# Kernel optimization log

Hardware: AMD Instinct MI355X
Metric: run time of the kernel (lower is better)

## Reference

```python
import jax, jax.numpy as jnp
import numpy as np

B, N, DIN = 16, 1024, 256
HEADS, OUT_DIM = 4, 256
F = OUT_DIM // HEADS  # per-head feature dim
NEG_SLOPE = 0.2
MASK_VAL = -1e9


def setup_inputs() -> dict:
    key = jax.random.key(0)
    k1, k2, k3, k4, k5, k6 = jax.random.split(key, 6)
    x = jax.random.normal(k1, (B, N, DIN), dtype=jnp.float32)
    adj = jax.random.uniform(k2, (B, N, N), dtype=jnp.float32)  # >0.5 -> edge
    # GATConv learned params (Glorot-ish scale)
    W = jax.random.normal(k3, (DIN, HEADS, F), dtype=jnp.float32) * (1.0 / np.sqrt(DIN))
    a_src = jax.random.normal(k4, (HEADS, F), dtype=jnp.float32) * (1.0 / np.sqrt(F))
    a_dst = jax.random.normal(k5, (HEADS, F), dtype=jnp.float32) * (1.0 / np.sqrt(F))
    bias = jax.random.normal(k6, (OUT_DIM,), dtype=jnp.float32) * 0.01
    return {"x": x, "adj": adj, "W": W, "a_src": a_src, "a_dst": a_dst, "bias": bias}


def reference(x, adj, W, a_src, a_dst, bias):
    # GAT over a dense adjacency mask: mathematically identical to
    # per-sample tf.where edge extraction + edge-list GATConv (softmax over
    # j with adj[b,i,j] > 0.5), but fully vectorized over the batch.
    b, n, _ = x.shape
    h = jnp.einsum('bnd,dhf->bnhf', x, W)                  # [B,N,H,F]
    e_src = jnp.einsum('bnhf,hf->bhn', h, a_src)           # source logits
    e_dst = jnp.einsum('bnhf,hf->bhn', h, a_dst)           # target logits
    # e[b,h,i,j]: edge j -> i
    e = e_dst[:, :, :, None] + e_src[:, :, None, :]        # [B,H,N,N]
    e = jax.nn.leaky_relu(e, NEG_SLOPE)
    mask = (adj > 0.5)[:, None, :, :]                      # [B,1,N,N]
    e = jnp.where(mask, e, MASK_VAL)
    attn = jax.nn.softmax(e, axis=-1)                      # softmax over sources j
    out = jnp.einsum('bhij,bjhf->bihf', attn, h)           # aggregate messages
    out = out.reshape(b, n, HEADS * F) + bias              # concat heads + bias
    return out
```

## Files before the change

### kernel.cpp

```cpp
#include <hip/hip_runtime.h>

#define B_    16
#define N_    1024
#define DIN_  256
#define H_    4
#define F_    64
#define COUT_ 256
#define NEG_  0.2f
#define LOG2E_ 1.4426950408889634f

typedef __bf16 bf16x8 __attribute__((ext_vector_type(8)));
typedef float  f32x4  __attribute__((ext_vector_type(4)));
typedef unsigned short u16x8 __attribute__((ext_vector_type(8)));
typedef unsigned short u16x4 __attribute__((ext_vector_type(4)));
typedef unsigned int   u32x4 __attribute__((ext_vector_type(4)));

__device__ __forceinline__ unsigned short f2bf(float f) {
    unsigned u = __builtin_bit_cast(unsigned, f);
    u += 0x7fffu + ((u >> 16) & 1u);
    return (unsigned short)(u >> 16);
}

__global__ __launch_bounds__(256) void prep_kernel(
    const float* __restrict__ W, unsigned short* __restrict__ Wtp) {
    const int c = blockIdx.x, k = threadIdx.x;
    const int w = c >> 6, ft = (c >> 4) & 3, l15 = c & 15;
    const int it = k >> 5, q = (k >> 3) & 3, jj = k & 7;
    const int ln = q * 16 + l15;
    Wtp[((((w * 8 + it) * 4 + ft) * 64) + ln) * 8 + jj] = f2bf(W[k * COUT_ + c]);
}

__global__ __launch_bounds__(256, 4) void stage_kernel(
    const float* __restrict__ adj, const float* __restrict__ x,
    const unsigned short* __restrict__ Wtp, const float* __restrict__ a_src,
    const float* __restrict__ a_dst, unsigned int* __restrict__ mask,
    unsigned short* __restrict__ hp, float* __restrict__ e_src,
    float* __restrict__ e_dst) {
    __shared__ unsigned short xs[16][264];
    const int w  = threadIdx.x >> 6;
    const int ln = threadIdx.x & 63;

    if (blockIdx.x < 4096) {
        const int row = blockIdx.x * 4 + w;
        const float* ar = adj + (size_t)row * N_ + ln * 4;

        f32x4 v0 = *(const f32x4*)(ar);
        f32x4 v1 = *(const f32x4*)(ar + 256);
        f32x4 v2 = *(const f32x4*)(ar + 512);
        f32x4 v3 = *(const f32x4*)(ar + 768);

        unsigned long long bal[4][4];
#pragma unroll
        for (int e = 0; e < 4; e++) {
            bal[0][e] = __ballot(v0[e] > 0.5f);
            bal[1][e] = __ballot(v1[e] > 0.5f);
            bal[2][e] = __ballot(v2[e] > 0.5f);
            bal[3][e] = __ballot(v3[e] > 0.5f);
        }

        const int c_ = (ln >> 3) & 3;
        const int sh = (ln & 7) * 8;
        unsigned wd = 0;
#pragma unroll
        for (int e = 0; e < 4; e++) {
            unsigned long long be = (c_ == 0) ? bal[0][e]
                                  : (c_ == 1) ? bal[1][e]
                                  : (c_ == 2) ? bal[2][e] : bal[3][e];
            wd |= ((unsigned)((be >> sh) & 0xffull)) << (8 * e);
        }
        if (ln < 32)
            mask[(size_t)row * 32 + ln] = wd;
    } else {
        const int blk = blockIdx.x - 4096;
        const int b   = blk & 15;
        const int it0 = (blk >> 4) * 16;
        const int l15 = ln & 15;
        const int q   = ln >> 4;

#pragma unroll
        for (int s = 0; s < 4; s++) {
            const int row = w * 4 + s;
            f32x4 xv = *(const f32x4*)(x + (size_t)(b * N_ + it0 + row) * DIN_ + ln * 4);
            unsigned lo = (unsigned)f2bf(xv[0]) | ((unsigned)f2bf(xv[1]) << 16);
            unsigned hi = (unsigned)f2bf(xv[2]) | ((unsigned)f2bf(xv[3]) << 16);
            unsigned long long hb = (unsigned long long)lo | ((unsigned long long)hi << 32);
            *(unsigned long long*)&xs[row][ln * 4] = hb;
        }
        __syncthreads();

        f32x4 acc[4];
#pragma unroll
        for (int ft = 0; ft < 4; ft++) acc[ft] = (f32x4)0.0f;

        const unsigned short* wb = Wtp + (w * 8) * 4 * 64 * 8 + ln * 8;
#pragma unroll
        for (int it = 0; it < 8; it++) {
            bf16x8 af = *(const bf16x8*)&xs[l15][it * 32 + q * 8];
#pragma unroll
            for (int ft = 0; ft < 4; ft++) {
                bf16x8 bf = *((const bf16x8*)(wb + (it * 4 + ft) * 512));
                acc[ft] = __builtin_amdgcn_mfma_f32_16x16x32_bf16(af, bf, acc[ft], 0, 0, 0);
            }
        }

        const int jg = it0 >> 5;
        const int q2 = 2 * ((it0 >> 4) & 1) + (q >> 1);
#pragma unroll
        for (int ft = 0; ft < 4; ft++) {
            u16x4 hb;
#pragma unroll
            for (int r = 0; r < 4; r++) hb[r] = f2bf(acc[ft][r]);
            const size_t addr =
                (size_t)((((b * H_ + w) * 32 + jg) * 4 + ft) * 64 + q2 * 16 + l15) * 8 + (q & 1) * 4;
            *((u16x4*)(hp + addr)) = hb;
        }

        float as_v[4], ad_v[4];
#pragma unroll
        for (int ft = 0; ft < 4; ft++) {
            as_v[ft] = a_src[w * F_ + ft * 16 + l15];
            ad_v[ft] = a_dst[w * F_ + ft * 16 + l15];
        }
        float ps[4], pd[4];
#pragma unroll
        for (int r = 0; r < 4; r++) {
            ps[r] = 0.0f; pd[r] = 0.0f;
#pragma unroll
            for (int ft = 0; ft < 4; ft++) {
                ps[r] += acc[ft][r] * as_v[ft];
                pd[r] += acc[ft][r] * ad_v[ft];
            }
        }
#pragma unroll
        for (int off = 1; off <= 8; off <<= 1)
#pragma unroll
            for (int r = 0; r < 4; r++) {
                ps[r] += __shfl_xor(ps[r], off);
                pd[r] += __shfl_xor(pd[r], off);
            }
        float vs = (l15 == 0) ? ps[0] : (l15 == 1) ? ps[1] : (l15 == 2) ? ps[2] : ps[3];
        float vd = (l15 == 0) ? pd[0] : (l15 == 1) ? pd[1] : (l15 == 2) ? pd[2] : pd[3];
        if (l15 < 4) {
            const int i = it0 + q * 4 + l15;
            e_src[(b * H_ + w) * N_ + i] = vs * LOG2E_;
            e_dst[(b * H_ + w) * N_ + i] = vd * LOG2E_;
        }
    }
}

__global__ __launch_bounds__(512, 4) void gat_attn_kernel(
    const unsigned int* __restrict__ mask, const unsigned short* __restrict__ hp,
    const float* __restrict__ e_src, const float* __restrict__ e_dst,
    const float* __restrict__ bias, float* __restrict__ out) {
    const int lid = ((blockIdx.x & 7) << 6) | (blockIdx.x >> 3);
    const int b   = lid >> 5;
    const int it0 = (lid & 31) * 32;
    const int w8  = threadIdx.x >> 6;
    const int h   = w8 & 3;
    const int jh  = w8 >> 2;
    const int ln  = threadIdx.x & 63;
    const int l15 = ln & 15;
    const int q   = ln >> 4;

    __shared__ float lds[H_][2][5][64][4];
    __shared__ float es_s[H_][N_];
    __shared__ unsigned mk_s[32][37];

    {
        const int tid = threadIdx.x;
#pragma unroll
        for (int p = 0; p < 2; p++) {
            const int c  = p * 512 + tid;
            const int h_ = c >> 8;
            const int of = (c & 255) * 4;
            *(f32x4*)&es_s[h_][of] =
                *(const f32x4*)(e_src + (size_t)(b * H_ + h_) * N_ + of);
        }
        if (tid < 256) {
            const int ii  = tid >> 3;
            const int jc4 = (tid & 7) * 4;
            u32x4 mv = *(const u32x4*)(mask + ((size_t)(b * N_ + it0 + ii)) * 32 + jc4);
            mk_s[ii][jc4 + 0] = mv[0];
            mk_s[ii][jc4 + 1] = mv[1];
            mk_s[ii][jc4 + 2] = mv[2];
            mk_s[ii][jc4 + 3] = mv[3];
        }
    }

    float edv[2];
    edv[0] = e_dst[(b * H_ + h) * N_ + it0 + l15];
    edv[1] = e_dst[(b * H_ + h) * N_ + it0 + 16 + l15];

    const unsigned short* hp_base = hp + (size_t)((b * H_ + h) * 32) * 2048 + ln * 8;

    f32x4 acc[2][4];
    f32x4 accs[2];
#pragma unroll
    for (int mt = 0; mt < 2; mt++) {
#pragma unroll
        for (int ft = 0; ft < 4; ft++) acc[mt][ft] = (f32x4)0.0f;
        accs[mt] = (f32x4)0.0f;
    }

    u16x8 ones_u;
#pragma unroll
    for (int jj = 0; jj < 8; jj++) ones_u[jj] = 0x3F80;
    const bf16x8 ones = __builtin_bit_cast(bf16x8, ones_u);

    __syncthreads();

    const unsigned short* hf0 = hp_base + (size_t)(jh * 16) * 2048;
    bf16x8 nb0 = *((const bf16x8*)(hf0 + 0 * 512));
    bf16x8 nb1 = *((const bf16x8*)(hf0 + 1 * 512));
    bf16x8 nb2 = *((const bf16x8*)(hf0 + 2 * 512));
    bf16x8 nb3 = *((const bf16x8*)(hf0 + 3 * 512));

    const int bp0[4] = {0, 16, 1, 17};
    const int bp1[4] = {8, 24, 9, 25};

#pragma unroll
    for (int t = 0; t < 16; t++) {
        const int jg = jh * 16 + t;
        const bf16x8 cb0 = nb0, cb1 = nb1, cb2 = nb2, cb3 = nb3;
        if (t < 15) {
            const unsigned short* hfn = hp_base + (size_t)(jg + 1) * 2048;
            nb0 = *((const bf16x8*)(hfn + 0 * 512));
            nb1 = *((const bf16x8*)(hfn + 1 * 512));
            nb2 = *((const bf16x8*)(hfn + 2 * 512));
            nb3 = *((const bf16x8*)(hfn + 3 * 512));
        }

        f32x4 e0 = *(const f32x4*)&es_s[h][jg * 32 + q * 8];
        f32x4 e1 = *(const f32x4*)&es_s[h][jg * 32 + q * 8 + 4];
        const unsigned w0 = mk_s[l15][jg] >> (2 * q);
        const unsigned w1 = mk_s[16 + l15][jg] >> (2 * q);

        float es8[8] = {e0[0], e0[1], e0[2], e0[3], e1[0], e1[1], e1[2], e1[3]};

        bf16x8 afr[2];
#pragma unroll
        for (int mt = 0; mt < 2; mt++) {
            const unsigned mw = mt ? w1 : w0;
            u32x4 up;
#pragma unroll
            for (int p2 = 0; p2 < 4; p2++) {
                float t0 = edv[mt] + es8[2 * p2];
                float t1 = edv[mt] + es8[2 * p2 + 1];
                t0 = fmaxf(t0, NEG_ * t0);
                t1 = fmaxf(t1, NEG_ * t1);
                float p0 = __builtin_amdgcn_exp2f(t0);
                float p1 = __builtin_amdgcn_exp2f(t1);
                p0 = ((mw >> bp0[p2]) & 1u) ? p0 : 0.0f;
                p1 = ((mw >> bp1[p2]) & 1u) ? p1 : 0.0f;
                up[p2] = __builtin_amdgcn_perm(__builtin_bit_cast(unsigned, p1),
                                               __builtin_bit_cast(unsigned, p0),
                                               0x07060302u);
            }
            afr[mt] = __builtin_bit_cast(bf16x8, up);
        }
#pragma unroll
        for (int mt = 0; mt < 2; mt++) {
            acc[mt][0] = __builtin_amdgcn_mfma_f32_16x16x32_bf16(afr[mt], cb0, acc[mt][0], 0, 0, 0);
            acc[mt][1] = __builtin_amdgcn_mfma_f32_16x16x32_bf16(afr[mt], cb1, acc[mt][1], 0, 0, 0);
            acc[mt][2] = __builtin_amdgcn_mfma_f32_16x16x32_bf16(afr[mt], cb2, acc[mt][2], 0, 0, 0);
            acc[mt][3] = __builtin_amdgcn_mfma_f32_16x16x32_bf16(afr[mt], cb3, acc[mt][3], 0, 0, 0);
            accs[mt]   = __builtin_amdgcn_mfma_f32_16x16x32_bf16(afr[mt], ones, accs[mt], 0, 0, 0);
        }
    }

    if (jh == 1) {
#pragma unroll
        for (int mt = 0; mt < 2; mt++) {
#pragma unroll
            for (int ft = 0; ft < 4; ft++)
                *(f32x4*)&lds[h][mt][ft][ln][0] = acc[mt][ft];
            *(f32x4*)&lds[h][mt][4][ln][0] = accs[mt];
        }
    }
    __syncthreads();
    if (jh == 0) {
#pragma unroll
        for (int mt = 0; mt < 2; mt++) {
#pragma unroll
            for (int ft = 0; ft < 4; ft++)
                acc[mt][ft] += *(const f32x4*)&lds[h][mt][ft][ln][0];
            accs[mt] += *(const f32x4*)&lds[h][mt][4][ln][0];
        }
        float bias_v[4];
#pragma unroll
        for (int ft = 0; ft < 4; ft++) bias_v[ft] = bias[h * F_ + ft * 16 + l15];
#pragma unroll
        for (int mt = 0; mt < 2; mt++) {
            f32x4 rinv;
#pragma unroll
            for (int r = 0; r < 4; r++) rinv[r] = 1.0f / accs[mt][r];
#pragma unroll
            for (int ft = 0; ft < 4; ft++)
#pragma unroll
                for (int r = 0; r < 4; r++) {
                    const int i = it0 + mt * 16 + q * 4 + r;
                    const int c = h * F_ + ft * 16 + l15;
                    out[(size_t)(b * N_ + i) * COUT_ + c] = acc[mt][ft][r] * rinv[r] + bias_v[ft];
                }
        }
    }
}

extern "C" void kernel_launch(void* const* d_in, const int* in_sizes, int n_in,
                              void* d_out, int out_size, void* d_ws, size_t ws_size,
                              hipStream_t stream) {
    const float* x     = (const float*)d_in[0];
    const float* adj   = (const float*)d_in[1];
    const float* W     = (const float*)d_in[2];
    const float* a_src = (const float*)d_in[3];
    const float* a_dst = (const float*)d_in[4];
    const float* bias  = (const float*)d_in[5];
    float* out = (float*)d_out;

    char* ws = (char*)d_ws;
    unsigned short* Wtp = (unsigned short*)ws;
    unsigned short* hp  = (unsigned short*)(ws + 131072);
    float* e_src        = (float*)(ws + 131072 + 8388608);
    float* e_dst        = (float*)(ws + 131072 + 8388608 + 262144);
    unsigned int* mask  = (unsigned int*)(ws + 131072 + 8388608 + 524288);

    prep_kernel<<<256, 256, 0, stream>>>(W, Wtp);
    stage_kernel<<<5120, 256, 0, stream>>>(adj, x, Wtp, a_src, a_dst, mask, hp, e_src, e_dst);
    gat_attn_kernel<<<512, 512, 0, stream>>>(mask, hp, e_src, e_dst, bias, out);
}
```

Before: 142.5 us.

## Fuse adjacency mask bit-packing into attention kernel, dropping mask buffer

Moves the adj>0.5 ballot packing out of the stage kernel and into the attention kernel's prologue. Each attention block reads its 32 adjacency rows directly and writes packed bits straight to shared memory. This removes the global mask write and re-read plus 4096 stage blocks. In exchange, the attention kernel now streams the 64MB adjacency itself before its barrier, which could expose load latency unless the prefetch of hp overlaps it.

New measurement: 145.2 us. No clear change (+1.9%).

```diff
diff --git a/kernel.cpp b/kernel.cpp
--- a/kernel.cpp
+++ b/kernel.cpp
@@ -31,125 +31,92 @@
 }
 
 __global__ __launch_bounds__(256, 4) void stage_kernel(
-    const float* __restrict__ adj, const float* __restrict__ x,
-    const unsigned short* __restrict__ Wtp, const float* __restrict__ a_src,
-    const float* __restrict__ a_dst, unsigned int* __restrict__ mask,
+    const float* __restrict__ x, const unsigned short* __restrict__ Wtp,
+    const float* __restrict__ a_src, const float* __restrict__ a_dst,
     unsigned short* __restrict__ hp, float* __restrict__ e_src,
     float* __restrict__ e_dst) {
     __shared__ unsigned short xs[16][264];
     const int w  = threadIdx.x >> 6;
     const int ln = threadIdx.x & 63;
 
-    if (blockIdx.x < 4096) {
-        const int row = blockIdx.x * 4 + w;
-        const float* ar = adj + (size_t)row * N_ + ln * 4;
-
-        f32x4 v0 = *(const f32x4*)(ar);
-        f32x4 v1 = *(const f32x4*)(ar + 256);
-        f32x4 v2 = *(const f32x4*)(ar + 512);
-        f32x4 v3 = *(const f32x4*)(ar + 768);
-
-        unsigned long long bal[4][4];
-#pragma unroll
-        for (int e = 0; e < 4; e++) {
-            bal[0][e] = __ballot(v0[e] > 0.5f);
-            bal[1][e] = __ballot(v1[e] > 0.5f);
-            bal[2][e] = __ballot(v2[e] > 0.5f);
-            bal[3][e] = __ballot(v3[e] > 0.5f);
-        }
-
-        const int c_ = (ln >> 3) & 3;
-        const int sh = (ln & 7) * 8;
-        unsigned wd = 0;
-#pragma unroll
-        for (int e = 0; e < 4; e++) {
-            unsigned long long be = (c_ == 0) ? bal[0][e]
-                                  : (c_ == 1) ? bal[1][e]
-                                  : (c_ == 2) ? bal[2][e] : bal[3][e];
-            wd |= ((unsigned)((be >> sh) & 0xffull)) << (8 * e);
-        }
-        if (ln < 32)
-            mask[(size_t)row * 32 + ln] = wd;
-    } else {
-        const int blk = blockIdx.x - 4096;
-        const int b   = blk & 15;
-        const int it0 = (blk >> 4) * 16;
-        const int l15 = ln & 15;
-        const int q   = ln >> 4;
-
-#pragma unroll
-        for (int s = 0; s < 4; s++) {
-            const int row = w * 4 + s;
-            f32x4 xv = *(const f32x4*)(x + (size_t)(b * N_ + it0 + row) * DIN_ + ln * 4);
-            unsigned lo = (unsigned)f2bf(xv[0]) | ((unsigned)f2bf(xv[1]) << 16);
-            unsigned hi = (unsigned)f2bf(xv[2]) | ((unsigned)f2bf(xv[3]) << 16);
-            unsigned long long hb = (unsigned long long)lo | ((unsigned long long)hi << 32);
-            *(unsigned long long*)&xs[row][ln * 4] = hb;
-        }
-        __syncthreads();
-
-        f32x4 acc[4];
-#pragma unroll
-        for (int ft = 0; ft < 4; ft++) acc[ft] = (f32x4)0.0f;
-
-        const unsigned short* wb = Wtp + (w * 8) * 4 * 64 * 8 + ln * 8;
-#pragma unroll
-        for (int it = 0; it < 8; it++) {
-            bf16x8 af = *(const bf16x8*)&xs[l15][it * 32 + q * 8];
-#pragma unroll
-            for (int ft = 0; ft < 4; ft++) {
-                bf16x8 bf = *((const bf16x8*)(wb + (it * 4 + ft) * 512));
-                acc[ft] = __builtin_amdgcn_mfma_f32_16x16x32_bf16(af, bf, acc[ft], 0, 0, 0);
-            }
-        }
-
-        const int jg = it0 >> 5;
-        const int q2 = 2 * ((it0 >> 4) & 1) + (q >> 1);
+    const int blk = blockIdx.x;
+    const int b   = blk & 15;
+    const int it0 = (blk >> 4) * 16;
+    const int l15 = ln & 15;
+    const int q   = ln >> 4;
+
+#pragma unroll
+    for (int s = 0; s < 4; s++) {
+        const int row = w * 4 + s;
+        f32x4 xv = *(const f32x4*)(x + (size_t)(b * N_ + it0 + row) * DIN_ + ln * 4);
+        unsigned lo = (unsigned)f2bf(xv[0]) | ((unsigned)f2bf(xv[1]) << 16);
+        unsigned hi = (unsigned)f2bf(xv[2]) | ((unsigned)f2bf(xv[3]) << 16);
+        unsigned long long hb = (unsigned long long)lo | ((unsigned long long)hi << 32);
+        *(unsigned long long*)&xs[row][ln * 4] = hb;
+    }
+    __syncthreads();
+
+    f32x4 acc[4];
+#pragma unroll
+    for (int ft = 0; ft < 4; ft++) acc[ft] = (f32x4)0.0f;
+
+    const unsigned short* wb = Wtp + (w * 8) * 4 * 64 * 8 + ln * 8;
+#pragma unroll
+    for (int it = 0; it < 8; it++) {
+        bf16x8 af = *(const bf16x8*)&xs[l15][it * 32 + q * 8];
 #pragma unroll
         for (int ft = 0; ft < 4; ft++) {
-            u16x4 hb;
-#pragma unroll
-            for (int r = 0; r < 4; r++) hb[r] = f2bf(acc[ft][r]);
-            const size_t addr =
-                (size_t)((((b * H_ + w) * 32 + jg) * 4 + ft) * 64 + q2 * 16 + l15) * 8 + (q & 1) * 4;
-            *((u16x4*)(hp + addr)) = hb;
-        }
-
-        float as_v[4], ad_v[4];
+            bf16x8 bf = *((const bf16x8*)(wb + (it * 4 + ft) * 512));
+            acc[ft] = __builtin_amdgcn_mfma_f32_16x16x32_bf16(af, bf, acc[ft], 0, 0, 0);
+        }
+    }
+
+    const int jg = it0 >> 5;
+    const int q2 = 2 * ((it0 >> 4) & 1) + (q >> 1);
+#pragma unroll
+    for (int ft = 0; ft < 4; ft++) {
+        u16x4 hb;
+#pragma unroll
+        for (int r = 0; r < 4; r++) hb[r] = f2bf(acc[ft][r]);
+        const size_t addr =
+            (size_t)((((b * H_ + w) * 32 + jg) * 4 + ft) * 64 + q2 * 16 + l15) * 8 + (q & 1) * 4;
+        *((u16x4*)(hp + addr)) = hb;
+    }
+
+    float as_v[4], ad_v[4];
+#pragma unroll
+    for (int ft = 0; ft < 4; ft++) {
+        as_v[ft] = a_src[w * F_ + ft * 16 + l15];
+        ad_v[ft] = a_dst[w * F_ + ft * 16 + l15];
+    }
+    float ps[4], pd[4];
+#pragma unroll
+    for (int r = 0; r < 4; r++) {
+        ps[r] = 0.0f; pd[r] = 0.0f;
 #pragma unroll
         for (int ft = 0; ft < 4; ft++) {
-            as_v[ft] = a_src[w * F_ + ft * 16 + l15];
-            ad_v[ft] = a_dst[w * F_ + ft * 16 + l15];
-        }
-        float ps[4], pd[4];
+            ps[r] += acc[ft][r] * as_v[ft];
+            pd[r] += acc[ft][r] * ad_v[ft];
+        }
+    }
+#pragma unroll
+    for (int off = 1; off <= 8; off <<= 1)
 #pragma unroll
         for (int r = 0; r < 4; r++) {
-            ps[r] = 0.0f; pd[r] = 0.0f;
-#pragma unroll
-            for (int ft = 0; ft < 4; ft++) {
-                ps[r] += acc[ft][r] * as_v[ft];
-                pd[r] += acc[ft][r] * ad_v[ft];
-            }
-        }
-#pragma unroll
-        for (int off = 1; off <= 8; off <<= 1)
-#pragma unroll
-            for (int r = 0; r < 4; r++) {
-                ps[r] += __shfl_xor(ps[r], off);
-                pd[r] += __shfl_xor(pd[r], off);
-            }
-        float vs = (l15 == 0) ? ps[0] : (l15 == 1) ? ps[1] : (l15 == 2) ? ps[2] : ps[3];
-        float vd = (l15 == 0) ? pd[0] : (l15 == 1) ? pd[1] : (l15 == 2) ? pd[2] : pd[3];
-        if (l15 < 4) {
-            const int i = it0 + q * 4 + l15;
-            e_src[(b * H_ + w) * N_ + i] = vs * LOG2E_;
-            e_dst[(b * H_ + w) * N_ + i] = vd * LOG2E_;
-        }
+            ps[r] += __shfl_xor(ps[r], off);
+            pd[r] += __shfl_xor(pd[r], off);
+        }
+    float vs = (l15 == 0) ? ps[0] : (l15 == 1) ? ps[1] : (l15 == 2) ? ps[2] : ps[3];
+    float vd = (l15 == 0) ? pd[0] : (l15 == 1) ? pd[1] : (l15 == 2) ? pd[2] : pd[3];
+    if (l15 < 4) {
+        const int i = it0 + q * 4 + l15;
+        e_src[(b * H_ + w) * N_ + i] = vs * LOG2E_;
+        e_dst[(b * H_ + w) * N_ + i] = vd * LOG2E_;
     }
 }
 
 __global__ __launch_bounds__(512, 4) void gat_attn_kernel(
-    const unsigned int* __restrict__ mask, const unsigned short* __restrict__ hp,
+    const float* __restrict__ adj, const unsigned short* __restrict__ hp,
     const float* __restrict__ e_src, const float* __restrict__ e_dst,
     const float* __restrict__ bias, float* __restrict__ out) {
     const int lid = ((blockIdx.x & 7) << 6) | (blockIdx.x >> 3);
@@ -176,14 +143,22 @@
             *(f32x4*)&es_s[h_][of] =
                 *(const f32x4*)(e_src + (size_t)(b * H_ + h_) * N_ + of);
         }
-        if (tid < 256) {
-            const int ii  = tid >> 3;
-            const int jc4 = (tid & 7) * 4;
-            u32x4 mv = *(const u32x4*)(mask + ((size_t)(b * N_ + it0 + ii)) * 32 + jc4);
-            mk_s[ii][jc4 + 0] = mv[0];
-            mk_s[ii][jc4 + 1] = mv[1];
-            mk_s[ii][jc4 + 2] = mv[2];
-            mk_s[ii][jc4 + 3] = mv[3];
+        const int r4 = ln >> 4;
+        const float* arow =
+            adj + (size_t)(b * N_ + it0 + w8 * 4 + r4) * N_ + l15 * 4;
+#pragma unroll 4
+        for (int it = 0; it < 16; it++) {
+            f32x4 v = *(const f32x4*)(arow + it * 64);
+            unsigned long long bal[4];
+#pragma unroll
+            for (int e = 0; e < 4; e++) bal[e] = __ballot(v[e] > 0.5f);
+            if (ln < 8) {
+                unsigned wd = 0;
+#pragma unroll
+                for (int e = 0; e < 4; e++)
+                    wd |= ((unsigned)((bal[e] >> (8 * ln)) & 0xffull)) << (8 * e);
+                mk_s[w8 * 4 + (ln >> 1)][2 * it + (ln & 1)] = wd;
+            }
         }
     }
 
@@ -206,14 +181,14 @@
 #pragma unroll
     for (int jj = 0; jj < 8; jj++) ones_u[jj] = 0x3F80;
     const bf16x8 ones = __builtin_bit_cast(bf16x8, ones_u);
-
-    __syncthreads();
 
     const unsigned short* hf0 = hp_base + (size_t)(jh * 16) * 2048;
     bf16x8 nb0 = *((const bf16x8*)(hf0 + 0 * 512));
     bf16x8 nb1 = *((const bf16x8*)(hf0 + 1 * 512));
     bf16x8 nb2 = *((const bf16x8*)(hf0 + 2 * 512));
     bf16x8 nb3 = *((const bf16x8*)(hf0 + 3 * 512));
+
+    __syncthreads();
 
     const int bp0[4] = {0, 16, 1, 17};
     const int bp1[4] = {8, 24, 9, 25};
@@ -322,9 +297,8 @@
     unsigned short* hp  = (unsigned short*)(ws + 131072);
     float* e_src        = (float*)(ws + 131072 + 8388608);
     float* e_dst        = (float*)(ws + 131072 + 8388608 + 262144);
-    unsigned int* mask  = (unsigned int*)(ws + 131072 + 8388608 + 524288);
 
     prep_kernel<<<256, 256, 0, stream>>>(W, Wtp);
-    stage_kernel<<<5120, 256, 0, stream>>>(adj, x, Wtp, a_src, a_dst, mask, hp, e_src, e_dst);
-    gat_attn_kernel<<<512, 512, 0, stream>>>(mask, hp, e_src, e_dst, bias, out);
-}
+    stage_kernel<<<1024, 256, 0, stream>>>(x, Wtp, a_src, a_dst, hp, e_src, e_dst);
+    gat_attn_kernel<<<512, 512, 0, stream>>>(adj, hp, e_src, e_dst, bias, out);
+}
```

## Coarsen adjacency mask blocks and interleave them with projection blocks

Applied to the files above, without the earlier changes.

Each mask-building block now handles 16 adjacency rows instead of 4, so every wave issues 16 vector loads up front before doing the ballots. Mask blocks and projection blocks are interleaved by the parity of the block index, which shrinks the grid from 5120 to 2048 blocks. The aim is more memory-level parallelism per wave on the bandwidth-bound 64 MB adjacency read, and better overlap of compute-heavy projection blocks with mask blocks. In exchange, register pressure rises and there are fewer blocks to balance across the GPU.

Result: no change. 143.6 us (+0.8%).

```diff
diff --git a/kernel.cpp b/kernel.cpp
--- a/kernel.cpp
+++ b/kernel.cpp
@@ -40,38 +40,43 @@
     const int w  = threadIdx.x >> 6;
     const int ln = threadIdx.x & 63;
 
-    if (blockIdx.x < 4096) {
-        const int row = blockIdx.x * 4 + w;
-        const float* ar = adj + (size_t)row * N_ + ln * 4;
-
-        f32x4 v0 = *(const f32x4*)(ar);
-        f32x4 v1 = *(const f32x4*)(ar + 256);
-        f32x4 v2 = *(const f32x4*)(ar + 512);
-        f32x4 v3 = *(const f32x4*)(ar + 768);
-
-        unsigned long long bal[4][4];
-#pragma unroll
-        for (int e = 0; e < 4; e++) {
-            bal[0][e] = __ballot(v0[e] > 0.5f);
-            bal[1][e] = __ballot(v1[e] > 0.5f);
-            bal[2][e] = __ballot(v2[e] > 0.5f);
-            bal[3][e] = __ballot(v3[e] > 0.5f);
-        }
-
-        const int c_ = (ln >> 3) & 3;
-        const int sh = (ln & 7) * 8;
-        unsigned wd = 0;
-#pragma unroll
-        for (int e = 0; e < 4; e++) {
-            unsigned long long be = (c_ == 0) ? bal[0][e]
-                                  : (c_ == 1) ? bal[1][e]
-                                  : (c_ == 2) ? bal[2][e] : bal[3][e];
-            wd |= ((unsigned)((be >> sh) & 0xffull)) << (8 * e);
-        }
-        if (ln < 32)
-            mask[(size_t)row * 32 + ln] = wd;
+    if ((blockIdx.x & 1) == 0) {
+        const int mblk = blockIdx.x >> 1;
+        const int row0 = mblk * 16 + w * 4;
+        const float* ar = adj + (size_t)row0 * N_ + ln * 4;
+
+        f32x4 v[4][4];
+#pragma unroll
+        for (int r = 0; r < 4; r++)
+#pragma unroll
+            for (int c = 0; c < 4; c++)
+                v[r][c] = *(const f32x4*)(ar + (size_t)r * N_ + c * 256);
+
+#pragma unroll
+        for (int r = 0; r < 4; r++) {
+            unsigned long long bal[4][4];
+#pragma unroll
+            for (int e = 0; e < 4; e++) {
+                bal[0][e] = __ballot(v[r][0][e] > 0.5f);
+                bal[1][e] = __ballot(v[r][1][e] > 0.5f);
+                bal[2][e] = __ballot(v[r][2][e] > 0.5f);
+                bal[3][e] = __ballot(v[r][3][e] > 0.5f);
+            }
+            const int c_ = (ln >> 3) & 3;
+            const int sh = (ln & 7) * 8;
+            unsigned wd = 0;
+#pragma unroll
+            for (int e = 0; e < 4; e++) {
+                unsigned long long be = (c_ == 0) ? bal[0][e]
+                                      : (c_ == 1) ? bal[1][e]
+                                      : (c_ == 2) ? bal[2][e] : bal[3][e];
+                wd |= ((unsigned)((be >> sh) & 0xffull)) << (8 * e);
+            }
+            if (ln < 32)
+                mask[(size_t)(row0 + r) * 32 + ln] = wd;
+        }
     } else {
-        const int blk = blockIdx.x - 4096;
+        const int blk = blockIdx.x >> 1;
         const int b   = blk & 15;
         const int it0 = (blk >> 4) * 16;
         const int l15 = ln & 15;
@@ -325,6 +330,6 @@
     unsigned int* mask  = (unsigned int*)(ws + 131072 + 8388608 + 524288);
 
     prep_kernel<<<256, 256, 0, stream>>>(W, Wtp);
-    stage_kernel<<<5120, 256, 0, stream>>>(adj, x, Wtp, a_src, a_dst, mask, hp, e_src, e_dst);
+    stage_kernel<<<2048, 256, 0, stream>>>(adj, x, Wtp, a_src, a_dst, mask, hp, e_src, e_dst);
     gat_attn_kernel<<<512, 512, 0, stream>>>(mask, hp, e_src, e_dst, bias, out);
 }
```
